# Kernel optimization log

Measured on AMD Instinct MI355X. Metric: run time of the kernel, lower is better.

Reference implementation:

```python
import jax, jax.numpy as jnp
import numpy as np

BN, L, DM = 2, 1024, 1024
D_STATE, D_CONV, EXPAND = 16, 4, 2
D_INNER = DM * EXPAND


def setup_inputs() -> dict:
    key = jax.random.key(0)
    ks = jax.random.split(key, 12)
    s = lambda fan: 1.0 / np.sqrt(fan)
    x = jax.random.normal(ks[0], (BN, L, DM), jnp.float32)
    in_w = jax.random.normal(ks[1], (DM, 2 * D_INNER), jnp.float32) * s(DM)
    in_b = jnp.zeros((2 * D_INNER,), jnp.float32)
    # depthwise conv kernel, flax layout (window, in_per_group=1, features)
    conv_w = jax.random.normal(ks[2], (D_CONV, 1, D_INNER), jnp.float32) * s(D_CONV)
    conv_b = jnp.zeros((D_INNER,), jnp.float32)
    # negative A for a stable scan (exp(dt*A) <= 1), as in real Mamba
    A = -jax.random.uniform(ks[3], (D_INNER, D_STATE), jnp.float32, 0.1, 1.0)
    Dp = jnp.ones((D_INNER,), jnp.float32)
    B_w = jax.random.normal(ks[4], (D_INNER, D_STATE), jnp.float32) * s(D_INNER)
    B_b = jnp.zeros((D_STATE,), jnp.float32)
    C_w = jax.random.normal(ks[5], (D_INNER, D_STATE), jnp.float32) * s(D_INNER)
    C_b = jnp.zeros((D_STATE,), jnp.float32)
    dt_w = jax.random.normal(ks[6], (D_INNER, D_INNER), jnp.float32) * s(D_INNER)
    dt_b = jnp.full((D_INNER,), -4.0, jnp.float32)  # softplus -> small dt
    out_w = jax.random.normal(ks[7], (D_INNER, DM), jnp.float32) * s(D_INNER)
    out_b = jnp.zeros((DM,), jnp.float32)
    return {"x": x, "in_w": in_w, "in_b": in_b, "conv_w": conv_w, "conv_b": conv_b,
            "A": A, "Dp": Dp, "B_w": B_w, "B_b": B_b, "C_w": C_w, "C_b": C_b,
            "dt_w": dt_w, "dt_b": dt_b, "out_w": out_w, "out_b": out_b}


def reference(x, in_w, in_b, conv_w, conv_b, A, Dp, B_w, B_b, C_w, C_b, dt_w, dt_b, out_w, out_b):
    Bn, Ln, _ = x.shape
    d_inner, d_state = A.shape
    xp = x @ in_w + in_b                      # [B,L,2*d_inner]
    x_z, gate = jnp.split(xp, 2, axis=-1)
    # depthwise causal-ish SAME conv along L
    x_conv = jax.lax.conv_general_dilated(
        x_z, conv_w, window_strides=(1,), padding='SAME',
        dimension_numbers=('NWC', 'WIO', 'NWC'), feature_group_count=d_inner) + conv_b
    x_conv = jax.nn.silu(x_conv)              # [B,L,d_inner]
    Bm = x_conv @ B_w + B_b                   # [B,L,d_state]
    Cm = x_conv @ C_w + C_b                   # [B,L,d_state]
    dt = jax.nn.softplus(x_conv @ dt_w + dt_b)  # [B,L,d_inner]
    dA = jnp.exp(dt[..., None] * A[None, None])     # [B,L,d_inner,d_state]
    dB = dt[..., None] * Bm[..., None, :]           # [B,L,d_inner,d_state]

    def scan_fn(h, inp):
        x_t, dA_t, dB_t, C_t = inp            # [B,d_inner], [B,d_inner,S]x2, [B,S]
        h = dA_t * h + dB_t * x_t[..., None]
        y_t = jnp.sum(h * C_t[:, None, :], axis=-1)  # [B,d_inner]
        return h, y_t

    h0 = jnp.zeros((Bn, d_inner, d_state), x.dtype)
    tm = lambda t: jnp.swapaxes(t, 0, 1)      # time-major
    _, y = jax.lax.scan(scan_fn, h0, (tm(x_conv), tm(dA), tm(dB), tm(Cm)))
    y = jnp.swapaxes(y, 0, 1)                 # [B,L,d_inner]
    y = y + x_conv * Dp
    y = y * jax.nn.silu(gate)
    return y @ out_w + out_b                  # [B,L,d_model]
```

## Files before the change

### kernel.cpp

```cpp
#include <hip/hip_runtime.h>
#include <hip/hip_bf16.h>
#include <math.h>

#define BN_   2
#define L_    1024
#define DM_   1024
#define DS_   16
#define DI_   2048
#define M_    (BN_ * L_)
#define NBC_  2176

typedef __attribute__((ext_vector_type(8))) short short8;
typedef __attribute__((ext_vector_type(4))) float f32x4;

__device__ __forceinline__ unsigned short f2b(float f) {
    union { float f; unsigned u; } x; x.f = f;
    unsigned r = x.u + 0x7fffu + ((x.u >> 16) & 1u);
    return (unsigned short)(r >> 16);
}
__device__ __forceinline__ float b2f(unsigned short u) {
    union { unsigned u; float f; } x; x.u = ((unsigned)u) << 16; return x.f;
}

__device__ __forceinline__ void gload_lds16(const unsigned short* g, unsigned short* l) {
    __builtin_amdgcn_global_load_lds(
        (const __attribute__((address_space(1))) void*)g,
        (__attribute__((address_space(3))) void*)l, 16, 0, 0);
}

__global__ __launch_bounds__(256) void cast_bf16(
    const float* __restrict__ in, unsigned short* __restrict__ out, int n)
{
    const int i = (blockIdx.x * 256 + threadIdx.x) * 4;
    if (i >= n) return;
    float4 v = *(const float4*)(in + i);
    ushort4 o; o.x = f2b(v.x); o.y = f2b(v.y); o.z = f2b(v.z); o.w = f2b(v.w);
    *(ushort4*)(out + i) = o;
}

__global__ __launch_bounds__(256) void transpose_cast(
    const float* __restrict__ in, unsigned short* __restrict__ out, int R, int C)
{
    __shared__ float t[32][33];
    const int bx = blockIdx.x * 32;
    const int by = blockIdx.y * 32;
    const int tx = threadIdx.x & 31;
    const int ty = (threadIdx.x >> 5) * 4;
    #pragma unroll
    for (int j = 0; j < 4; ++j)
        t[ty + j][tx] = in[(size_t)(by + ty + j) * C + bx + tx];
    __syncthreads();
    #pragma unroll
    for (int j = 0; j < 4; ++j)
        out[(size_t)(bx + ty + j) * R + by + tx] = f2b(t[tx][ty + j]);
}

__global__ __launch_bounds__(256) void bc_pack(
    const float* __restrict__ Bw, const float* __restrict__ Cw,
    unsigned short* __restrict__ w2)
{
    const int idx = blockIdx.x * 256 + threadIdx.x;
    const int r = idx >> 11;
    const int k = idx & 2047;
    const float* src = (r < 16) ? Bw : Cw;
    w2[(size_t)(2048 + r) * 2048 + k] = f2b(src[k * 16 + (r & 15)]);
}

template<int BM, int BN, int MODE>
__global__ __launch_bounds__(256) void gemm_mfma(
    const unsigned short* __restrict__ A,
    const unsigned short* __restrict__ Bt,
    const float* __restrict__ b0, const float* __restrict__ b1,
    const float* __restrict__ b2,
    float* __restrict__ F0, float* __restrict__ F1, float* __restrict__ F2,
    unsigned short* __restrict__ U0, unsigned short* __restrict__ U1,
    int M, int N, int K, int NS)
{
    constexpr int MF  = BM / 32;
    constexpr int NF  = BN / 32;
    constexpr int ACW = BM / 32;
    constexpr int BCW = BN / 32;

    __shared__ unsigned short Asl[2][BM * 64];
    __shared__ unsigned short Bsl[2][BN * 64];

    const int tid  = threadIdx.x;
    const int wave = tid >> 6;
    const int lane = tid & 63;

    const int gx  = gridDim.x, gy = gridDim.y;
    const int bid = blockIdx.y * gx + blockIdx.x;
    const int q   = (gx * gy) >> 3;
    const int nb  = (bid & 7) * q + (bid >> 3);
    const int by  = nb % gy;
    const int bx  = nb / gy;

    const int row0 = by * BM;
    const int col0 = bx * BN;
    const int wr   = (wave >> 1) * (BM / 2);
    const int wc   = (wave & 1) * (BN / 2);

    const int srow = lane >> 3;
    const int scol = ((lane & 7) ^ (lane >> 3)) * 8;

    auto stage = [&](int buf, int kt) {
        #pragma unroll
        for (int i = 0; i < ACW; ++i) {
            const int ch = wave * ACW + i;
            gload_lds16(A + (size_t)(row0 + ch * 8 + srow) * K + kt + scol,
                        &Asl[buf][ch * 512]);
        }
        #pragma unroll
        for (int i = 0; i < BCW; ++i) {
            const int ch = wave * BCW + i;
            gload_lds16(Bt + (size_t)(col0 + ch * 8 + srow) * K + kt + scol,
                        &Bsl[buf][ch * 512]);
        }
    };

    f32x4 acc[MF][NF];
    #pragma unroll
    for (int m = 0; m < MF; ++m)
        #pragma unroll
        for (int n = 0; n < NF; ++n)
            acc[m][n] = (f32x4){0.f, 0.f, 0.f, 0.f};

    stage(0, 0);
    __syncthreads();

    const int nk = K >> 6;
    int cur = 0;
    for (int kt = 0; kt < nk; ++kt) {
        if (kt + 1 < nk) stage(cur ^ 1, (kt + 1) << 6);

        short8 af[MF][2], bf[NF][2];
        const int lrow  = lane & 15;
        const int xsw   = (lane & 7) * 8;
        const int cbase = (lane >> 4) * 8;
        #pragma unroll
        for (int m = 0; m < MF; ++m)
            #pragma unroll
            for (int kk = 0; kk < 2; ++kk)
                af[m][kk] = *(const short8*)
                    &Asl[cur][(wr + m * 16 + lrow) * 64 + ((kk * 32 + cbase) ^ xsw)];
        #pragma unroll
        for (int n = 0; n < NF; ++n)
            #pragma unroll
            for (int kk = 0; kk < 2; ++kk)
                bf[n][kk] = *(const short8*)
                    &Bsl[cur][(wc + n * 16 + lrow) * 64 + ((kk * 32 + cbase) ^ xsw)];

        #pragma unroll
        for (int m = 0; m < MF; ++m)
            #pragma unroll
            for (int n = 0; n < NF; ++n) {
                acc[m][n] = __builtin_amdgcn_mfma_f32_16x16x32_bf16(
                    af[m][0], bf[n][0], acc[m][n], 0, 0, 0);
                acc[m][n] = __builtin_amdgcn_mfma_f32_16x16x32_bf16(
                    af[m][1], bf[n][1], acc[m][n], 0, 0, 0);
            }
        __syncthreads();
        cur ^= 1;
    }

    const int crow = (lane >> 4) * 4;
    const int ccol = lane & 15;
    #pragma unroll
    for (int m = 0; m < MF; ++m)
        #pragma unroll
        for (int n = 0; n < NF; ++n) {
            const int c = col0 + wc + n * 16 + ccol;
            if (MODE == 0) {
                const float bv = b0[c];
                unsigned short* dst = (c < NS) ? (U0 + c) : (U1 + (c - NS));
                #pragma unroll
                for (int j = 0; j < 4; ++j) {
                    const int r = row0 + wr + m * 16 + crow + j;
                    dst[(size_t)r * NS] = f2b(acc[m][n][j] + bv);
                }
            } else if (MODE == 1) {
                if (c < 2048) {
                    const float bv = b0[c];
                    #pragma unroll
                    for (int j = 0; j < 4; ++j) {
                        const int r = row0 + wr + m * 16 + crow + j;
                        float v = acc[m][n][j] + bv;
                        v = (v > 20.0f) ? v : log1pf(__expf(v));
                        F0[(size_t)r * 2048 + c] = v;
                    }
                } else if (c < 2064) {
                    const float bv = b1[c - 2048];
                    #pragma unroll
                    for (int j = 0; j < 4; ++j) {
                        const int r = row0 + wr + m * 16 + crow + j;
                        F1[(size_t)r * 16 + (c - 2048)] = acc[m][n][j] + bv;
                    }
                } else if (c < 2080) {
                    const float bv = b2[c - 2064];
                    #pragma unroll
                    for (int j = 0; j < 4; ++j) {
                        const int r = row0 + wr + m * 16 + crow + j;
                        F2[(size_t)r * 16 + (c - 2064)] = acc[m][n][j] + bv;
                    }
                }
            } else {
                const float bv = b0[c];
                #pragma unroll
                for (int j = 0; j < 4; ++j) {
                    const int r = row0 + wr + m * 16 + crow + j;
                    F0[(size_t)r * NS + c] = acc[m][n][j] + bv;
                }
            }
        }
}

__global__ __launch_bounds__(256) void conv_silu(
    const unsigned short* __restrict__ xzb, const float* __restrict__ cw,
    const float* __restrict__ cb, unsigned short* __restrict__ xcb)
{
    const int idx = blockIdx.x * 256 + threadIdx.x;
    if (idx >= BN_ * L_ * DI_) return;
    const int d = idx & (DI_ - 1);
    const int t = (idx / DI_) & (L_ - 1);
    const int b = idx / (DI_ * L_);

    float acc = cb[d];
    #pragma unroll
    for (int w = 0; w < 4; ++w) {
        const int tt = t + w - 1;
        if (tt >= 0 && tt < L_)
            acc = fmaf(b2f(xzb[((size_t)(b * L_ + tt)) * DI_ + d]), cw[w * DI_ + d], acc);
    }
    const float s = acc / (1.0f + __expf(-acc));
    xcb[idx] = f2b(s);
}

#define NCH_ 32
#define TL_  (L_ / NCH_)

__global__ __launch_bounds__(256) void scan_part1(
    const float* __restrict__ dt, const unsigned short* __restrict__ xcb,
    const float* __restrict__ Bm, const float* __restrict__ A,
    float* __restrict__ Pc, float* __restrict__ Hc)
{
    const int tid = threadIdx.x;
    const int d   = blockIdx.x * 256 + tid;
    const int b   = blockIdx.y;
    const int j   = blockIdx.z;
    const int t0  = j * TL_;

    __shared__ float s_Bm[TL_ * DS_];
    {
        const float* src = Bm + ((size_t)b * L_ + t0) * DS_;
        s_Bm[tid]       = src[tid];
        s_Bm[256 + tid] = src[256 + tid];
    }
    float a[DS_];
    #pragma unroll
    for (int qq = 0; qq < 4; ++qq)
        *(float4*)&a[qq * 4] = *(const float4*)(A + (size_t)d * DS_ + qq * 4);
    __syncthreads();

    const float* dtp = dt + ((size_t)b * L_ + t0) * DI_ + d;
    const unsigned short* xcp = xcb + ((size_t)b * L_ + t0) * DI_ + d;

    float h[DS_] = {};
    float P[DS_];
    #pragma unroll
    for (int s = 0; s < DS_; ++s) P[s] = 1.0f;

    float dtv = dtp[0], xcv = b2f(xcp[0]);
    #pragma unroll 4
    for (int t = 0; t < TL_; ++t) {
        float dtv_n = 0.f, xcv_n = 0.f;
        if (t + 1 < TL_) {
            dtv_n = dtp[(size_t)(t + 1) * DI_];
            xcv_n = b2f(xcp[(size_t)(t + 1) * DI_]);
        }
        const float dx = dtv * xcv;
        #pragma unroll
        for (int qq = 0; qq < 4; ++qq) {
            const float4 bm = *(const float4*)&s_Bm[t * DS_ + qq * 4];
            #pragma unroll
            for (int i = 0; i < 4; ++i) {
                const int s = qq * 4 + i;
                const float bv = (i == 0) ? bm.x : (i == 1) ? bm.y : (i == 2) ? bm.z : bm.w;
                const float dA = __expf(dtv * a[s]);
                P[s] *= dA;
                h[s] = fmaf(dA, h[s], dx * bv);
            }
        }
        dtv = dtv_n; xcv = xcv_n;
    }
    const size_t o0 = (((size_t)b * NCH_ + j) * DS_) * DI_ + d;
    #pragma unroll
    for (int s = 0; s < DS_; ++s) {
        Pc[o0 + (size_t)s * DI_] = P[s];
        Hc[o0 + (size_t)s * DI_] = h[s];
    }
}

__global__ __launch_bounds__(256) void scan_combine(
    const float* __restrict__ Pc, float* __restrict__ Hc)
{
    const size_t idx = (size_t)blockIdx.x * 256 + threadIdx.x;
    const size_t b   = idx / (DS_ * DI_);
    const size_t rem = idx % (DS_ * DI_);
    const size_t base   = b * ((size_t)NCH_ * DS_ * DI_) + rem;
    const size_t stride = (size_t)DS_ * DI_;
    float h = 0.f;
    #pragma unroll
    for (int j = 0; j < NCH_; ++j) {
        const size_t o = base + (size_t)j * stride;
        const float P  = Pc[o];
        const float hl = Hc[o];
        Hc[o] = h;
        h = fmaf(P, h, hl);
    }
}

__global__ __launch_bounds__(256) void scan_part2(
    const float* __restrict__ dt, const unsigned short* __restrict__ xcb,
    const unsigned short* __restrict__ gate,
    const float* __restrict__ Bm, const float* __restrict__ Cm,
    const float* __restrict__ A, const float* __restrict__ Dp,
    const float* __restrict__ Hin, unsigned short* __restrict__ ygb)
{
    const int tid = threadIdx.x;
    const int d   = blockIdx.x * 256 + tid;
    const int b   = blockIdx.y;
    const int j   = blockIdx.z;
    const int t0  = j * TL_;

    __shared__ float s_Bm[TL_ * DS_];
    __shared__ float s_Cm[TL_ * DS_];
    {
        const float* bsrc = Bm + ((size_t)b * L_ + t0) * DS_;
        const float* csrc = Cm + ((size_t)b * L_ + t0) * DS_;
        s_Bm[tid]       = bsrc[tid];
        s_Bm[256 + tid] = bsrc[256 + tid];
        s_Cm[tid]       = csrc[tid];
        s_Cm[256 + tid] = csrc[256 + tid];
    }
    float a[DS_];
    #pragma unroll
    for (int qq = 0; qq < 4; ++qq)
        *(float4*)&a[qq * 4] = *(const float4*)(A + (size_t)d * DS_ + qq * 4);
    const float dp = Dp[d];

    float h[DS_];
    {
        const size_t o0 = (((size_t)b * NCH_ + j) * DS_) * DI_ + d;
        #pragma unroll
        for (int s = 0; s < DS_; ++s) h[s] = Hin[o0 + (size_t)s * DI_];
    }
    __syncthreads();

    const size_t rbase = ((size_t)b * L_ + t0) * DI_ + d;
    const float* dtp = dt   + rbase;
    const unsigned short* xcp = xcb + rbase;
    const unsigned short* gvp = gate + rbase;
    unsigned short* yp = ygb + rbase;

    float dtv = dtp[0], xcv = b2f(xcp[0]), gv = b2f(gvp[0]);
    #pragma unroll 4
    for (int t = 0; t < TL_; ++t) {
        float dtv_n = 0.f, xcv_n = 0.f, gv_n = 0.f;
        if (t + 1 < TL_) {
            dtv_n = dtp[(size_t)(t + 1) * DI_];
            xcv_n = b2f(xcp[(size_t)(t + 1) * DI_]);
            gv_n  = b2f(gvp[(size_t)(t + 1) * DI_]);
        }
        const float dx = dtv * xcv;
        float y0 = 0.f, y1 = 0.f, y2 = 0.f, y3 = 0.f;
        #pragma unroll
        for (int qq = 0; qq < 4; ++qq) {
            const float4 bm = *(const float4*)&s_Bm[t * DS_ + qq * 4];
            const float4 cm = *(const float4*)&s_Cm[t * DS_ + qq * 4];
            #pragma unroll
            for (int i = 0; i < 4; ++i) {
                const int s = qq * 4 + i;
                const float bv = (i == 0) ? bm.x : (i == 1) ? bm.y : (i == 2) ? bm.z : bm.w;
                const float cv = (i == 0) ? cm.x : (i == 1) ? cm.y : (i == 2) ? cm.z : cm.w;
                const float dA = __expf(dtv * a[s]);
                h[s] = fmaf(dA, h[s], dx * bv);
                if (i == 0) y0 = fmaf(h[s], cv, y0);
                else if (i == 1) y1 = fmaf(h[s], cv, y1);
                else if (i == 2) y2 = fmaf(h[s], cv, y2);
                else y3 = fmaf(h[s], cv, y3);
            }
        }
        float y = (y0 + y1) + (y2 + y3);
        y = fmaf(xcv, dp, y);
        const float r = y * (gv / (1.0f + __expf(-gv)));
        yp[(size_t)t * DI_] = f2b(r);
        dtv = dtv_n; xcv = xcv_n; gv = gv_n;
    }
}

extern "C" void kernel_launch(void* const* d_in, const int* in_sizes, int n_in,
                              void* d_out, int out_size, void* d_ws, size_t ws_size,
                              hipStream_t stream)
{
    const float* x      = (const float*)d_in[0];
    const float* in_w   = (const float*)d_in[1];
    const float* in_b   = (const float*)d_in[2];
    const float* conv_w = (const float*)d_in[3];
    const float* conv_b = (const float*)d_in[4];
    const float* A      = (const float*)d_in[5];
    const float* Dp     = (const float*)d_in[6];
    const float* B_w    = (const float*)d_in[7];
    const float* B_b    = (const float*)d_in[8];
    const float* C_w    = (const float*)d_in[9];
    const float* C_b    = (const float*)d_in[10];
    const float* dt_w   = (const float*)d_in[11];
    const float* dt_b   = (const float*)d_in[12];
    const float* out_w  = (const float*)d_in[13];
    const float* out_b  = (const float*)d_in[14];
    float* out = (float*)d_out;

    float* dtb  = (float*)d_ws;
    float* Bm   = dtb + (size_t)M_ * DI_;
    float* Cm   = Bm  + (size_t)M_ * DS_;
    unsigned short* w3  = (unsigned short*)(Cm + (size_t)M_ * DS_);
    unsigned short* w1  = w3  + (size_t)DM_ * DI_;
    unsigned short* xb  = w1  + (size_t)2 * DI_ * DM_;
    unsigned short* w2  = xb  + (size_t)M_ * DM_;
    unsigned short* xcb = w2  + (size_t)NBC_ * DI_;
    unsigned short* xzb = xcb + (size_t)M_ * DI_;
    unsigned short* gtb = xzb + (size_t)M_ * DI_;
    unsigned short* ygb = xcb;
    float* Pc = (float*)w1;
    float* Hc = (float*)xb;

    cast_bf16<<<(M_ * DM_ / 4 + 255) / 256, 256, 0, stream>>>(x, xb, M_ * DM_);
    transpose_cast<<<dim3(2 * DI_ / 32, DM_ / 32), 256, 0, stream>>>(in_w, w1, DM_, 2 * DI_);

    gemm_mfma<64, 128, 0><<<dim3(2 * DI_ / 128, M_ / 64), 256, 0, stream>>>(
        xb, w1, in_b, nullptr, nullptr,
        nullptr, nullptr, nullptr, xzb, gtb, M_, 2 * DI_, DM_, DI_);

    conv_silu<<<(BN_ * L_ * DI_) / 256, 256, 0, stream>>>(xzb, conv_w, conv_b, xcb);

    transpose_cast<<<dim3(DI_ / 32, DI_ / 32), 256, 0, stream>>>(dt_w, w2, DI_, DI_);
    bc_pack<<<(32 * 2048) / 256, 256, 0, stream>>>(B_w, C_w, w2);

    gemm_mfma<64, 128, 1><<<dim3(NBC_ / 128, M_ / 64), 256, 0, stream>>>(
        xcb, w2, dt_b, B_b, C_b,
        dtb, Bm, Cm, nullptr, nullptr, M_, NBC_, DI_, NBC_);

    transpose_cast<<<dim3(DM_ / 32, DI_ / 32), 256, 0, stream>>>(out_w, w3, DI_, DM_);

    scan_part1<<<dim3(DI_ / 256, BN_, NCH_), 256, 0, stream>>>(
        dtb, xcb, Bm, A, Pc, Hc);
    scan_combine<<<(BN_ * DI_ * DS_) / 256, 256, 0, stream>>>(Pc, Hc);
    scan_part2<<<dim3(DI_ / 256, BN_, NCH_), 256, 0, stream>>>(
        dtb, xcb, gtb, Bm, Cm, A, Dp, Hc, ygb);

    gemm_mfma<64, 64, 2><<<dim3(DM_ / 64, M_ / 64), 256, 0, stream>>>(
        ygb, w3, out_b, nullptr, nullptr,
        out, nullptr, nullptr, nullptr, nullptr, M_, DM_, DI_, DM_);
}
```

Baseline: 193.9 us.

## Merge weight prep into one kernel and store dt as bf16

Folds the input cast, the three weight transpose-casts and the B/C pack into a single prep kernel, replacing five launches with one. It also has the dt GEMM epilogue write softplus(dt) as bf16 instead of fp32, and both scan kernels now read bf16 dt, which halves dt traffic. The cost is lower precision for dt inside the scan, which could affect accuracy.

```diff
diff --git a/kernel.cpp b/kernel.cpp
--- a/kernel.cpp
+++ b/kernel.cpp
@@ -28,22 +28,11 @@
         (__attribute__((address_space(3))) void*)l, 16, 0, 0);
 }
 
-__global__ __launch_bounds__(256) void cast_bf16(
-    const float* __restrict__ in, unsigned short* __restrict__ out, int n)
-{
-    const int i = (blockIdx.x * 256 + threadIdx.x) * 4;
-    if (i >= n) return;
-    float4 v = *(const float4*)(in + i);
-    ushort4 o; o.x = f2b(v.x); o.y = f2b(v.y); o.z = f2b(v.z); o.w = f2b(v.w);
-    *(ushort4*)(out + i) = o;
-}
-
-__global__ __launch_bounds__(256) void transpose_cast(
-    const float* __restrict__ in, unsigned short* __restrict__ out, int R, int C)
+__device__ __forceinline__ void tr_tile(
+    const float* __restrict__ in, unsigned short* __restrict__ out,
+    int R, int C, int bx, int by)
 {
     __shared__ float t[32][33];
-    const int bx = blockIdx.x * 32;
-    const int by = blockIdx.y * 32;
     const int tx = threadIdx.x & 31;
     const int ty = (threadIdx.x >> 5) * 4;
     #pragma unroll
@@ -55,15 +44,39 @@
         out[(size_t)(bx + ty + j) * R + by + tx] = f2b(t[tx][ty + j]);
 }
 
-__global__ __launch_bounds__(256) void bc_pack(
+__global__ __launch_bounds__(256) void prep(
+    const float* __restrict__ x,
+    const float* __restrict__ in_w, const float* __restrict__ dt_w,
+    const float* __restrict__ out_w,
     const float* __restrict__ Bw, const float* __restrict__ Cw,
-    unsigned short* __restrict__ w2)
-{
-    const int idx = blockIdx.x * 256 + threadIdx.x;
-    const int r = idx >> 11;
-    const int k = idx & 2047;
-    const float* src = (r < 16) ? Bw : Cw;
-    w2[(size_t)(2048 + r) * 2048 + k] = f2b(src[k * 16 + (r & 15)]);
+    unsigned short* __restrict__ xb, unsigned short* __restrict__ w1,
+    unsigned short* __restrict__ w2, unsigned short* __restrict__ w3)
+{
+    const int blk = blockIdx.x;
+    const int tid = threadIdx.x;
+    if (blk < 2048) {
+        const int i = (blk * 256 + tid) * 4;
+        if (i < M_ * DM_) {
+            float4 v = *(const float4*)(x + i);
+            ushort4 o; o.x = f2b(v.x); o.y = f2b(v.y); o.z = f2b(v.z); o.w = f2b(v.w);
+            *(ushort4*)(xb + i) = o;
+        }
+    } else if (blk < 6144) {
+        const int id = blk - 2048;
+        tr_tile(in_w, w1, DM_, 2 * DI_, (id & 127) * 32, (id >> 7) * 32);
+    } else if (blk < 10240) {
+        const int id = blk - 6144;
+        tr_tile(dt_w, w2, DI_, DI_, (id & 63) * 32, (id >> 6) * 32);
+    } else if (blk < 12288) {
+        const int id = blk - 10240;
+        tr_tile(out_w, w3, DI_, DM_, (id & 31) * 32, (id >> 5) * 32);
+    } else {
+        const int idx = (blk - 12288) * 256 + tid;
+        const int r = idx >> 11;
+        const int k = idx & 2047;
+        const float* src = (r < 16) ? Bw : Cw;
+        w2[(size_t)(2048 + r) * 2048 + k] = f2b(src[k * 16 + (r & 15)]);
+    }
 }
 
 template<int BM, int BN, int MODE>
@@ -186,7 +199,7 @@
                         const int r = row0 + wr + m * 16 + crow + j;
                         float v = acc[m][n][j] + bv;
                         v = (v > 20.0f) ? v : log1pf(__expf(v));
-                        F0[(size_t)r * 2048 + c] = v;
+                        U0[(size_t)r * 2048 + c] = f2b(v);
                     }
                 } else if (c < 2064) {
                     const float bv = b1[c - 2048];
@@ -239,7 +252,7 @@
 #define TL_  (L_ / NCH_)
 
 __global__ __launch_bounds__(256) void scan_part1(
-    const float* __restrict__ dt, const unsigned short* __restrict__ xcb,
+    const unsigned short* __restrict__ dt, const unsigned short* __restrict__ xcb,
     const float* __restrict__ Bm, const float* __restrict__ A,
     float* __restrict__ Pc, float* __restrict__ Hc)
 {
@@ -261,7 +274,7 @@
         *(float4*)&a[qq * 4] = *(const float4*)(A + (size_t)d * DS_ + qq * 4);
     __syncthreads();
 
-    const float* dtp = dt + ((size_t)b * L_ + t0) * DI_ + d;
+    const unsigned short* dtp = dt + ((size_t)b * L_ + t0) * DI_ + d;
     const unsigned short* xcp = xcb + ((size_t)b * L_ + t0) * DI_ + d;
 
     float h[DS_] = {};
@@ -269,12 +282,12 @@
     #pragma unroll
     for (int s = 0; s < DS_; ++s) P[s] = 1.0f;
 
-    float dtv = dtp[0], xcv = b2f(xcp[0]);
+    float dtv = b2f(dtp[0]), xcv = b2f(xcp[0]);
     #pragma unroll 4
     for (int t = 0; t < TL_; ++t) {
         float dtv_n = 0.f, xcv_n = 0.f;
         if (t + 1 < TL_) {
-            dtv_n = dtp[(size_t)(t + 1) * DI_];
+            dtv_n = b2f(dtp[(size_t)(t + 1) * DI_]);
             xcv_n = b2f(xcp[(size_t)(t + 1) * DI_]);
         }
         const float dx = dtv * xcv;
@@ -320,7 +333,7 @@
 }
 
 __global__ __launch_bounds__(256) void scan_part2(
-    const float* __restrict__ dt, const unsigned short* __restrict__ xcb,
+    const unsigned short* __restrict__ dt, const unsigned short* __restrict__ xcb,
     const unsigned short* __restrict__ gate,
     const float* __restrict__ Bm, const float* __restrict__ Cm,
     const float* __restrict__ A, const float* __restrict__ Dp,
@@ -357,17 +370,17 @@
     __syncthreads();
 
     const size_t rbase = ((size_t)b * L_ + t0) * DI_ + d;
-    const float* dtp = dt   + rbase;
-    const unsigned short* xcp = xcb + rbase;
+    const unsigned short* dtp = dt   + rbase;
+    const unsigned short* xcp = xcb  + rbase;
     const unsigned short* gvp = gate + rbase;
     unsigned short* yp = ygb + rbase;
 
-    float dtv = dtp[0], xcv = b2f(xcp[0]), gv = b2f(gvp[0]);
+    float dtv = b2f(dtp[0]), xcv = b2f(xcp[0]), gv = b2f(gvp[0]);
     #pragma unroll 4
     for (int t = 0; t < TL_; ++t) {
         float dtv_n = 0.f, xcv_n = 0.f, gv_n = 0.f;
         if (t + 1 < TL_) {
-            dtv_n = dtp[(size_t)(t + 1) * DI_];
+            dtv_n = b2f(dtp[(size_t)(t + 1) * DI_]);
             xcv_n = b2f(xcp[(size_t)(t + 1) * DI_]);
             gv_n  = b2f(gvp[(size_t)(t + 1) * DI_]);
         }
@@ -419,8 +432,8 @@
     const float* out_b  = (const float*)d_in[14];
     float* out = (float*)d_out;
 
-    float* dtb  = (float*)d_ws;
-    float* Bm   = dtb + (size_t)M_ * DI_;
+    unsigned short* dtb = (unsigned short*)d_ws;
+    float* Bm   = (float*)(dtb + (size_t)M_ * DI_);
     float* Cm   = Bm  + (size_t)M_ * DS_;
     unsigned short* w3  = (unsigned short*)(Cm + (size_t)M_ * DS_);
     unsigned short* w1  = w3  + (size_t)DM_ * DI_;
@@ -433,8 +446,7 @@
     float* Pc = (float*)w1;
     float* Hc = (float*)xb;
 
-    cast_bf16<<<(M_ * DM_ / 4 + 255) / 256, 256, 0, stream>>>(x, xb, M_ * DM_);
-    transpose_cast<<<dim3(2 * DI_ / 32, DM_ / 32), 256, 0, stream>>>(in_w, w1, DM_, 2 * DI_);
+    prep<<<12544, 256, 0, stream>>>(x, in_w, dt_w, out_w, B_w, C_w, xb, w1, w2, w3);
 
     gemm_mfma<64, 128, 0><<<dim3(2 * DI_ / 128, M_ / 64), 256, 0, stream>>>(
         xb, w1, in_b, nullptr, nullptr,
@@ -442,14 +454,9 @@
 
     conv_silu<<<(BN_ * L_ * DI_) / 256, 256, 0, stream>>>(xzb, conv_w, conv_b, xcb);
 
-    transpose_cast<<<dim3(DI_ / 32, DI_ / 32), 256, 0, stream>>>(dt_w, w2, DI_, DI_);
-    bc_pack<<<(32 * 2048) / 256, 256, 0, stream>>>(B_w, C_w, w2);
-
     gemm_mfma<64, 128, 1><<<dim3(NBC_ / 128, M_ / 64), 256, 0, stream>>>(
         xcb, w2, dt_b, B_b, C_b,
-        dtb, Bm, Cm, nullptr, nullptr, M_, NBC_, DI_, NBC_);
-
-    transpose_cast<<<dim3(DM_ / 32, DI_ / 32), 256, 0, stream>>>(out_w, w3, DI_, DM_);
+        nullptr, Bm, Cm, dtb, nullptr, M_, NBC_, DI_, NBC_);
 
     scan_part1<<<dim3(DI_ / 256, BN_, NCH_), 256, 0, stream>>>(
         dtb, xcb, Bm, A, Pc, Hc);
```

After: 182.8 us. 1.06x faster.
